# Optimization experiments

Measured on AMD Instinct MI355X. Metric: run time of the kernel, lower is better.

Reference implementation:

```python
import jax, jax.numpy as jnp
import numpy as np
from jax import lax

E = 10        # embed_dim
SEQ = 4000    # input_frame (sample_length=40)
G = 800       # group
F = 5         # frames_in_group
B = 16
VOCAB = 8192


def _conv2d(x, w, b):
    # x: [B, C, H, W], w: [O, I, 3, 3], padding=1 -> SAME
    y = lax.conv_general_dilated(x, w, (1, 1), 'SAME',
                                 dimension_numbers=('NCHW', 'OIHW', 'NCHW'))
    return y + b[None, :, None, None]


def _conv1d_k1(x, w, b):
    # Conv1d(seq, seq, kernel=1): x [B, S, L], w [S_out, S_in]
    return jnp.einsum('oi,bil->bol', w, x) + b[None, :, None]


def _linear(x, w, b):
    # torch Linear: w [out, in]
    return x @ w.T + b


def setup_inputs() -> dict:
    key = jax.random.key(0)
    ks = jax.random.split(key, 24)
    s = 0.02
    inp = {
        'X': jax.random.randint(ks[0], (B, SEQ, 15), 0, VOCAB),
        'emb_table': jax.random.normal(ks[1], (VOCAB, E), jnp.float32),
        'w_dwc_lsp': jax.random.normal(ks[2], (G, G, 3, 3), jnp.float32) * s,
        'b_dwc_lsp': jnp.zeros((G,), jnp.float32),
        'w_dwc_other': jax.random.normal(ks[3], (G, G, 3, 3), jnp.float32) * s,
        'b_dwc_other': jnp.zeros((G,), jnp.float32),
        'w_local': jax.random.normal(ks[4], (SEQ, SEQ), jnp.float32) * s,
        'b_local': jnp.zeros((SEQ,), jnp.float32),
        'w_global': jax.random.normal(ks[5], (SEQ, SEQ), jnp.float32) * s,
        'b_global': jnp.zeros((SEQ,), jnp.float32),
        'w_gq': jax.random.normal(ks[6], (4 * E, 4 * E), jnp.float32) * s,
        'b_gq': jnp.zeros((4 * E,), jnp.float32),
        'w_cq': jax.random.normal(ks[7], (4 * E, 4 * E), jnp.float32) * s,
        'b_cq': jnp.zeros((4 * E,), jnp.float32),
        'w_pq': jax.random.normal(ks[8], (4 * E, 3 * E), jnp.float32) * s,
        'b_pq': jnp.zeros((4 * E,), jnp.float32),
        'w_lk': jax.random.normal(ks[9], (4 * E, 4 * E), jnp.float32) * s,
        'b_lk': jnp.zeros((4 * E,), jnp.float32),
        'w_lv': jax.random.normal(ks[10], (4 * E, 4 * E), jnp.float32) * s,
        'b_lv': jnp.zeros((4 * E,), jnp.float32),
        'w_cls': jax.random.normal(ks[11], (1, SEQ * 4 * E * 3), jnp.float32) * 0.001,
        'b_cls': jnp.zeros((1,), jnp.float32),
        'bn_w': jnp.ones((1,), jnp.float32),
        'bn_b': jnp.zeros((1,), jnp.float32),
    }
    return inp


def reference(X, emb_table, w_dwc_lsp, b_dwc_lsp, w_dwc_other, b_dwc_other,
              w_local, b_local, w_global, b_global,
              w_gq, b_gq, w_cq, b_cq, w_pq, b_pq,
              w_lk, b_lk, w_lv, b_lv, w_cls, b_cls, bn_w, bn_b):
    batch, seq, cw = X.shape
    gamma = jnp.float32(0.8)
    pk = jnp.array([0, 0, 0, 0, 1, 3, 1, 2, 3, 2, 3, 1, 2, 3, 3], jnp.float32)
    D = jnp.repeat(gamma ** pk, E)  # [150]

    Xe = emb_table[X].reshape(batch, seq, cw * E) * D  # [B, S, 150]
    ch = Xe.reshape(batch, seq, cw, E)                  # 15 chunks of E

    lsp = ch[:, :, jnp.array([0, 1, 2, 3])].reshape(batch, seq, 4 * E)
    pitch = ch[:, :, jnp.array([4, 5, 10])].reshape(batch, seq, 3 * E)
    code = ch[:, :, jnp.array([6, 7, 11, 12])].reshape(batch, seq, 4 * E)
    gain = ch[:, :, jnp.array([8, 13, 9, 14])].reshape(batch, seq, 4 * E)

    conv_lsp = _conv2d(lsp.reshape(batch, G, F, 4 * E), w_dwc_lsp, b_dwc_lsp).reshape(batch, seq, 4 * E)
    conv_pitch = _conv2d(pitch.reshape(batch, G, F, 3 * E), w_dwc_other, b_dwc_other).reshape(batch, seq, 3 * E)
    conv_code = _conv2d(code.reshape(batch, G, F, 4 * E), w_dwc_other, b_dwc_other).reshape(batch, seq, 4 * E)
    conv_gain = _conv2d(gain.reshape(batch, G, F, 4 * E), w_dwc_other, b_dwc_other).reshape(batch, seq, 4 * E)

    conv_lsp = _conv1d_k1(conv_lsp, w_local, b_local)
    conv_pitch = _conv1d_k1(conv_pitch, w_local, b_local)
    conv_code = _conv1d_k1(conv_code, w_local, b_local)
    conv_gain = _conv1d_k1(conv_gain, w_local, b_local)

    gain_q = _linear(conv_gain, w_gq, b_gq)    # [B, S, 40]
    pitch_q = _linear(conv_pitch, w_pq, b_pq)  # [B, S, 40]
    code_q = _linear(conv_code, w_cq, b_cq)    # [B, S, 40]
    lsp_k = _linear(conv_lsp, w_lk, b_lk)
    lsp_v = _linear(conv_lsp, w_lv, b_lv)

    # Q @ K^T @ V with no softmax: associate as Q @ (K^T V), O(S*d^2)
    kv = jnp.einsum('bsd,bse->bde', lsp_k, lsp_v)  # [B, 40, 40]
    out_gain = jnp.einsum('bsd,bde->bse', gain_q, kv) + lsp
    out_pitch = jnp.einsum('bsd,bde->bse', pitch_q, kv) + lsp
    out_code = jnp.einsum('bsd,bde->bse', code_q, kv) + lsp

    atten_out = jnp.concatenate([out_gain, out_pitch, out_code], -1)  # [B, S, 120]
    gf = _conv1d_k1(atten_out, w_global, b_global).reshape(batch, -1)  # [B, 480000]

    y = gf @ w_cls.T + b_cls  # [B, 1]
    # BatchNorm1d(1) in eval mode: running_mean=0, running_var=1
    eps = jnp.float32(1e-5)
    y = y * (bn_w / jnp.sqrt(1.0 + eps)) + bn_b
    return jax.nn.sigmoid(y)
```

## Files before the change

kernel.cpp:

```cpp
#include <hip/hip_runtime.h>
#include <hip/hip_bf16.h>

typedef _Float16 f16;
typedef __attribute__((ext_vector_type(8))) _Float16 half8;
typedef __attribute__((ext_vector_type(4))) _Float16 half4;
typedef __attribute__((ext_vector_type(4))) float f32x4;

static const int BN = 16, SEQN = 4000;

__device__ __forceinline__ void gload_lds(f16* lds, const f16* g) {
  __builtin_amdgcn_global_load_lds((const __attribute__((address_space(1))) unsigned int*)g,
                                   (__attribute__((address_space(3))) unsigned int*)lds, 16, 0, 0);
}

__device__ __forceinline__ int xcd_swz(int orig, int nwg) {
  int q = nwg >> 3, r = nwg & 7, x = orig & 7, o = orig >> 3;
  return (x < r ? x * (q + 1) : r * (q + 1) + (x - r) * q) + o;
}

__global__ __launch_bounds__(256) void k_prepA(
    const float* __restrict__ w_dwc_l, f16* __restrict__ wp_lsp,
    const float* __restrict__ w_local, f16* __restrict__ wlp,
    const float* __restrict__ w_cls, f16* __restrict__ wcT) {
  __shared__ float sh[7200];
  int bid = blockIdx.x, t = threadIdx.x;
  if (bid < 800) {
    int o = bid;
    for (int p = t; p < 7200; p += 256) sh[p] = w_dwc_l[(long)o * 7200 + p];
    __syncthreads();
    for (int p = t; p < 7296; p += 256) {
      int seg = p / 2432, r = p - seg * 2432;
      f16 v = (f16)0.f;
      if (r < 2400) { int de = r / 800, gi = r % 800; v = (f16)sh[gi * 9 + seg * 3 + de]; }
      wp_lsp[(long)o * 7296 + p] = v;
    }
  } else if (bid < 4800) {
    int s = bid - 800;
    for (int p = t; p < 4000; p += 256) sh[p] = w_local[(long)s * 4000 + p];
    __syncthreads();
    for (int p = t; p < 4096; p += 256) {
      f16 v = (f16)0.f;
      if (p < 4000) { int f = p / 800, g = p % 800; v = (f16)sh[g * 5 + f]; }
      wlp[(long)s * 4096 + p] = v;
    }
  } else {
    int id = bid - 4800;
    int c0 = (id % 4) * 32, r0 = (id / 4) * 32;
    int tx = t & 31, ty = t >> 5;
    float (*tile)[33] = (float(*)[33])sh;
    for (int i = ty; i < 32; i += 8) {
      int r = r0 + i, c = c0 + tx;
      tile[i][tx] = (r < 4000 && c < 120) ? w_cls[(long)r * 120 + c] : 0.f;
    }
    __syncthreads();
    for (int i = ty; i < 32; i += 8) {
      int c = c0 + i, r = r0 + tx;
      if (c < 128 && r < 4000) wcT[(long)c * 4000 + r] = (f16)(tile[tx][i] * 1024.f);
    }
  }
}

__global__ __launch_bounds__(256) void k_pack_woT(const float* __restrict__ in,
                                                  f16* __restrict__ out) {
  __shared__ float sh[32][289];
  int bg = blockIdx.x % 25, bgi = blockIdx.x / 25;
  int g0 = bg * 32, gi0 = bgi * 32;
  int t = threadIdx.x;
  for (int p = t; p < 32 * 288; p += 256) {
    int gl = p / 288, q = p % 288;
    sh[gl][q] = in[(long)(g0 + gl) * 7200 + gi0 * 9 + q];
  }
  __syncthreads();
  for (int p = t; p < 9 * 32 * 32; p += 256) {
    int gl = p & 31, q = p >> 5;
    int gil = q & 31, z = q >> 5;
    out[(long)z * 640000 + (gi0 + gil) * 800 + g0 + gl] = (f16)sh[gl][gil * 9 + z];
  }
}

__global__ __launch_bounds__(256) void k_gather(
    const int* __restrict__ X, const float* __restrict__ emb,
    f16* __restrict__ P_lsp, f16* __restrict__ P_pit,
    f16* __restrict__ P_cod, f16* __restrict__ P_gai,
    float* __restrict__ lsp32) {
  __shared__ int sx_[2400];
  __shared__ float slsp[6400];
  const float scale[15] = {1.f,1.f,1.f,1.f,0.8f,0.512f,0.8f,0.64f,0.512f,0.64f,0.512f,0.8f,0.64f,0.512f,0.512f};
  const int br[15] = {0,0,0,0,1,1,2,2,3,3,1,2,2,3,3};
  const int po[15] = {0,1,2,3,0,1,0,1,0,2,2,2,3,1,3};
  int bid = blockIdx.x, t = threadIdx.x;
  int b = bid / 25, gc = bid % 25;
  int g0 = gc * 32, s0 = g0 * 5;
  const int* xbase = X + ((long)b * SEQN + s0) * 15;
  for (int p = t; p < 2400; p += 256) sx_[p] = xbase[p];
  __syncthreads();
  for (int it = t; it < 2400; it += 256) {
    int gl = it & 31, q = it >> 5, f = q % 5, c = q / 5;
    int idx = sx_[(gl * 5 + f) * 15 + c];
    const float* er = emb + (long)idx * 10;
    int ty = br[c], p = po[c];
    f16* P = (ty == 0) ? P_lsp : (ty == 1) ? P_pit : (ty == 2) ? P_cod : P_gai;
    int Wp = (ty == 1) ? 32 : 42;
    f16* base = P + ((long)((f + 1) * 16 + b) * Wp + (1 + p * 10)) * 800 + g0 + gl;
    float sc = scale[c];
#pragma unroll
    for (int j = 0; j < 10; j++) {
      float v = er[j] * sc;
      base[(long)j * 800] = (f16)v;
      if (ty == 0) slsp[(gl * 5 + f) * 40 + p * 10 + j] = v;
    }
  }
  __syncthreads();
  float* ldst = lsp32 + ((long)b * SEQN + s0) * 40;
  for (int p = t; p < 6400; p += 256) ldst[p] = slsp[p];
}

__global__ __launch_bounds__(256) void k_c1(const float* __restrict__ wcls,
                                            const float* __restrict__ bg, float* __restrict__ c1p) {
  __shared__ float red[256];
  int t = threadIdx.x;
  float s = 0.f;
  for (long i = (long)blockIdx.x * 256 + t; i < 480000; i += (long)120 * 256)
    s += wcls[i] * bg[i / 120];
  red[t] = s; __syncthreads();
  for (int o = 128; o > 0; o >>= 1) { if (t < o) red[t] += red[t + o]; __syncthreads(); }
  if (t == 0) c1p[blockIdx.x] = red[0];
}

__global__ __launch_bounds__(256) void k_gemm_conv(
    const f16* __restrict__ P, const f16* __restrict__ wp, float* __restrict__ Cp) {
  __shared__ __align__(16) f16 As[2][4096];
  __shared__ __align__(16) f16 Bs[2][4096];
  int lin = xcd_swz(blockIdx.x, 175);
  int nx = lin % 7, my = lin / 7;
  int m0 = my * 128, n0 = nx * 128;
  int z = blockIdx.y;
  int df = z >> 1, hf = z & 1;
  Cp += (long)z * 3200 * 800;
  int t = threadIdx.x;
  int gslot = (t & 3) ^ ((t >> 3) & 3);
  const f16 *ap[2], *bp[2];
#pragma unroll
  for (int q = 0; q < 2; q++) {
    int row = q * 64 + (t >> 2);
    int m = m0 + row;
    int f = m / 640, rem = m % 640, b = rem / 40, e = rem % 40;
    ap[q] = P + ((long)((f + df) * 16 + b) * 42 + e) * 800 + hf * 1216 + gslot * 8;
    bp[q] = wp + (long)(n0 + row) * 7296 + df * 2432 + hf * 1216 + gslot * 8;
  }
  int lane = t & 63, wv = t >> 6, l15 = lane & 15, kg = lane >> 4;
  int wm = (wv >> 1) * 64, wn = (wv & 1) * 64;
  int so = (kg ^ ((l15 >> 1) & 3)) << 3;
  f32x4 acc[4][4] = {};
  gload_lds(&As[0][t * 8], ap[0]); gload_lds(&As[0][2048 + t * 8], ap[1]);
  gload_lds(&Bs[0][t * 8], bp[0]); gload_lds(&Bs[0][2048 + t * 8], bp[1]);
  __syncthreads();
  int cur = 0;
  for (int kt = 0; kt < 38; kt++) {
    if (kt + 1 < 38) {
      int o = (kt + 1) * 32, nb = cur ^ 1;
      gload_lds(&As[nb][t * 8], ap[0] + o); gload_lds(&As[nb][2048 + t * 8], ap[1] + o);
      gload_lds(&Bs[nb][t * 8], bp[0] + o); gload_lds(&Bs[nb][2048 + t * 8], bp[1] + o);
    }
    half8 av[4], bv[4];
#pragma unroll
    for (int i = 0; i < 4; i++) av[i] = *(const half8*)&As[cur][(wm + i * 16 + l15) * 32 + so];
#pragma unroll
    for (int j = 0; j < 4; j++) bv[j] = *(const half8*)&Bs[cur][(wn + j * 16 + l15) * 32 + so];
#pragma unroll
    for (int i = 0; i < 4; i++)
#pragma unroll
      for (int j = 0; j < 4; j++)
        acc[i][j] = __builtin_amdgcn_mfma_f32_16x16x32_f16(av[i], bv[j], acc[i][j], 0, 0, 0);
    __syncthreads();
    cur ^= 1;
  }
#pragma unroll
  for (int i = 0; i < 4; i++) {
    int mb = m0 + wm + i * 16 + kg * 4;
#pragma unroll
    for (int j = 0; j < 4; j++) {
      int n = n0 + wn + j * 16 + l15;
      if (n >= 800) continue;
      f32x4 d = acc[i][j];
#pragma unroll
      for (int r = 0; r < 4; r++)
        Cp[(long)(mb + r) * 800 + n] = d[r];
    }
  }
}

__global__ void k_co_reduce(const float* __restrict__ Cp, const float* __restrict__ bias,
                            f16* __restrict__ co) {
  int id = blockIdx.x * blockDim.x + threadIdx.x;
  if (id >= 640000) return;
  int m = id / 200, n4 = (id % 200) * 4;
  long o = (long)m * 800 + n4;
  f32x4 s = *(const f32x4*)&bias[n4];
#pragma unroll
  for (int z = 0; z < 6; z++) s += *(const f32x4*)&Cp[(long)z * 2560000 + o];
  int f = m / 640, r2 = m % 640;
  half4 h = {(f16)s[0], (f16)s[1], (f16)s[2], (f16)s[3]};
  *(half4*)&co[(long)r2 * 4000 + f * 800 + n4] = h;
}

__global__ __launch_bounds__(256) void k_gemm128(
    const f16* __restrict__ A, int lda, const f16* __restrict__ Bm, int ldb,
    float* __restrict__ C, int ldc,
    int gx, int nwg, int nkt, int KTtot, long cslice, long az, long bz, long cz,
    int Mreal, int Nreal, int Aclamp) {
  __shared__ __align__(16) f16 As[2][4096];
  __shared__ __align__(16) f16 Bs[2][4096];
  A += (long)blockIdx.z * az;
  Bm += (long)blockIdx.z * bz;
  C += (long)blockIdx.z * cz + (long)blockIdx.y * cslice;
  int lin = xcd_swz(blockIdx.x, nwg);
  int nx = lin % gx, my = lin / gx;
  int m0 = my * 128, n0 = nx * 128;
  int kt0 = blockIdx.y * nkt;
  int ktn = nkt; if (kt0 + ktn > KTtot) ktn = KTtot - kt0;
  int t = threadIdx.x;
  int gslot = (t & 3) ^ ((t >> 3) & 3);
  const f16 *ap[2], *bp[2];
#pragma unroll
  for (int q = 0; q < 2; q++) {
    int row = q * 64 + (t >> 2);
    int ra = m0 + row; if (ra >= Aclamp) ra = Aclamp - 1;
    ap[q] = A + (long)ra * lda + (long)kt0 * 32 + gslot * 8;
    bp[q] = Bm + (long)(n0 + row) * ldb + (long)kt0 * 32 + gslot * 8;
  }
  int lane = t & 63, wv = t >> 6, l15 = lane & 15, kg = lane >> 4;
  int wm = (wv >> 1) * 64, wn = (wv & 1) * 64;
  int so = (kg ^ ((l15 >> 1) & 3)) << 3;
  f32x4 acc[4][4] = {};
  gload_lds(&As[0][t * 8], ap[0]); gload_lds(&As[0][2048 + t * 8], ap[1]);
  gload_lds(&Bs[0][t * 8], bp[0]); gload_lds(&Bs[0][2048 + t * 8], bp[1]);
  __syncthreads();
  int cur = 0;
  for (int kt = 0; kt < ktn; kt++) {
    if (kt + 1 < ktn) {
      int o = (kt + 1) * 32, nb = cur ^ 1;
      gload_lds(&As[nb][t * 8], ap[0] + o); gload_lds(&As[nb][2048 + t * 8], ap[1] + o);
      gload_lds(&Bs[nb][t * 8], bp[0] + o); gload_lds(&Bs[nb][2048 + t * 8], bp[1] + o);
    }
    half8 av[4], bv[4];
#pragma unroll
    for (int i = 0; i < 4; i++) av[i] = *(const half8*)&As[cur][(wm + i * 16 + l15) * 32 + so];
#pragma unroll
    for (int j = 0; j < 4; j++) bv[j] = *(const half8*)&Bs[cur][(wn + j * 16 + l15) * 32 + so];
#pragma unroll
    for (int i = 0; i < 4; i++)
#pragma unroll
      for (int j = 0; j < 4; j++)
        acc[i][j] = __builtin_amdgcn_mfma_f32_16x16x32_f16(av[i], bv[j], acc[i][j], 0, 0, 0);
    __syncthreads();
    cur ^= 1;
  }
#pragma unroll
  for (int i = 0; i < 4; i++) {
    int mb = m0 + wm + i * 16 + kg * 4;
#pragma unroll
    for (int j = 0; j < 4; j++) {
      int n = n0 + wn + j * 16 + l15;
      if (n >= Nreal) continue;
      f32x4 d = acc[i][j];
#pragma unroll
      for (int r = 0; r < 4; r++) {
        int m = mb + r;
        if (m >= Mreal) continue;
        C[(long)m * ldc + n] = d[r];
      }
    }
  }
}

__global__ __launch_bounds__(256) void k_gemm_tn(
    const f16* __restrict__ A, int lda, const float* __restrict__ B, int ldb,
    float* __restrict__ C, int ldc, int nkt, int KTtot, long cslice,
    int Mreal, int Nreal) {
  __shared__ __align__(16) f16 As[4096];
  __shared__ __align__(16) f16 Bs[128 * 36];
  int n0 = blockIdx.x * 128;
  int kt0 = blockIdx.y * nkt;
  int ktn = nkt; if (kt0 + ktn > KTtot) ktn = KTtot - kt0;
  C += (long)blockIdx.y * cslice;
  int t = threadIdx.x;
  int gslot = (t & 3) ^ ((t >> 3) & 3);
  const f16 *ap0, *ap1;
  {
    int r0 = t >> 2, r1 = 64 + (t >> 2);
    if (r0 >= Mreal) r0 = Mreal - 1;
    if (r1 >= Mreal) r1 = Mreal - 1;
    ap0 = A + (long)r0 * lda + (long)kt0 * 32 + gslot * 8;
    ap1 = A + (long)r1 * lda + (long)kt0 * 32 + gslot * 8;
  }
  int lane = t & 63, wv = t >> 6;
  int wm = (wv >> 1) * 64, wn = (wv & 1) * 64;
  int l15 = lane & 15, kg = lane >> 4;
  int so = (kg ^ ((l15 >> 1) & 3)) << 3;
  f32x4 acc[4][4] = {};
  for (int kt = 0; kt < ktn; kt++) {
    float rb[4][4];
    int nli[4], kqi[4];
#pragma unroll
    for (int i = 0; i < 4; i++) {
      int id = i * 256 + t;
      nli[i] = id & 127; kqi[i] = id >> 7;
      int gn = n0 + nli[i]; if (gn >= Nreal) gn = Nreal - 1;
      long kb = ((long)(kt0 + kt) * 32 + kqi[i] * 4);
#pragma unroll
      for (int j = 0; j < 4; j++) rb[i][j] = B[(kb + j) * ldb + gn];
    }
    __syncthreads();
    gload_lds(&As[t * 8], ap0 + kt * 32);
    gload_lds(&As[2048 + t * 8], ap1 + kt * 32);
#pragma unroll
    for (int i = 0; i < 4; i++) {
      half4 h = {(f16)rb[i][0], (f16)rb[i][1], (f16)rb[i][2], (f16)rb[i][3]};
      *(half4*)&Bs[nli[i] * 36 + kqi[i] * 4] = h;
    }
    __syncthreads();
    half8 av[4], bv[4];
#pragma unroll
    for (int i = 0; i < 4; i++) {
      av[i] = *(const half8*)(&As[(wm + i * 16 + l15) * 32 + so]);
      bv[i] = *(const half8*)(&Bs[(wn + i * 16 + l15) * 36 + kg * 8]);
    }
#pragma unroll
    for (int i = 0; i < 4; i++)
#pragma unroll
      for (int j = 0; j < 4; j++)
        acc[i][j] = __builtin_amdgcn_mfma_f32_16x16x32_f16(av[i], bv[j], acc[i][j], 0, 0, 0);
  }
#pragma unroll
  for (int i = 0; i < 4; i++) {
    int mb = wm + i * 16 + kg * 4;
#pragma unroll
    for (int j = 0; j < 4; j++) {
      int n = n0 + wn + j * 16 + l15;
      if (n >= Nreal) continue;
      f32x4 d = acc[i][j];
#pragma unroll
      for (int r = 0; r < 4; r++) {
        int m = mb + r;
        if (m >= Mreal) continue;
        C[(long)m * ldc + n] = d[r];
      }
    }
  }
}

template <int MODE>
__global__ __launch_bounds__(128) void k_vredT2(const float* __restrict__ vp,
                                                float* __restrict__ vout,
                                                f16* __restrict__ tout) {
  int s = blockIdx.x * 128 + threadIdx.x;
  int ec = blockIdx.y;
  if (s >= 4000) return;
  int g = s / 5, f = s % 5;
  float sums[40];
#pragma unroll
  for (int eo = 0; eo < 40; eo++) {
    int e = ec * 40 + eo;
    float sum = 0.f;
#pragma unroll
    for (int z = 0; z < 10; z++) sum += vp[(long)z * 480000 + (long)e * 4000 + s];
    sums[eo] = sum;
    if (MODE == 0) tout[(long)e * 4000 + s] = (f16)sum;
    else tout[(long)(f * 120 + e) * 832 + g] = (f16)sum;
  }
#pragma unroll
  for (int q = 0; q < 10; q++)
    *(f32x4*)&vout[(long)s * 120 + ec * 40 + q * 4] = *(f32x4*)&sums[q * 4];
}

__global__ void k_cl_reduce(const float* __restrict__ Clp, const float* __restrict__ bl,
                            float* __restrict__ cl) {
  int id = blockIdx.x * blockDim.x + threadIdx.x;
  if (id >= 640000) return;
  int m = id / 160, n4 = (id % 160) * 4;
  long o = (long)m * 640 + n4;
  f32x4 s = {0.f, 0.f, 0.f, 0.f};
#pragma unroll
  for (int z = 0; z < 6; z++) s += *(const f32x4*)&Clp[(long)z * 2560000 + o];
  float b = bl[m];
  s += (f32x4){b, b, b, b};
  *(f32x4*)&cl[o] = s;
}

__global__ void k_fold_bp(const float* __restrict__ A9, f16* __restrict__ Bp) {
  int id = blockIdx.x * blockDim.x + threadIdx.x;
  if (id >= 7 * 120 * 2496) return;
  int fp = id / 299520;
  int r = id % 299520;
  int eg = r / 2496, k2 = r % 2496;
  int zk = k2 / 832, kk = k2 % 832;
  if (kk >= 800) { Bp[id] = (f16)0.f; return; }
  float s = 0.f;
#pragma unroll
  for (int dh = 0; dh < 3; dh++) {
    int f = fp - dh;
    if (f >= 0 && f < 5)
      s += A9[((long)(dh * 3 + zk) * 640 + f * 120 + eg) * 800 + kk];
  }
  Bp[id] = (f16)s;
}

__global__ __launch_bounds__(256) void k_gemm_u(
    const f16* __restrict__ Pg, const f16* __restrict__ Pp, const f16* __restrict__ Pc,
    const f16* __restrict__ Bp, float* __restrict__ Upart) {
  __shared__ __align__(16) f16 As[2][4096];
  __shared__ __align__(16) f16 Bs[2][4096];
  int m0 = blockIdx.x * 64;
  int y = blockIdx.y, fp = y / 3, zk = y % 3;
  const f16* P; int seg0, jw, Wp, e0;
  if (m0 < 640)       { seg0 = 0;    jw = 40; Wp = 42; e0 = 0;  P = Pg; }
  else if (m0 < 1152) { seg0 = 640;  jw = 30; Wp = 32; e0 = 40; P = Pp; }
  else                { seg0 = 1152; jw = 40; Wp = 42; e0 = 80; P = Pc; }
  P += (long)fp * 16 * Wp * 800;
  int t = threadIdx.x;
  int gslot = (t & 7) ^ ((t >> 3) & 7);
  const f16 *ap[2], *bp[2];
#pragma unroll
  for (int q = 0; q < 2; q++) {
    int row = q * 32 + (t >> 3);
    int l = m0 + row - seg0; if (l >= 16 * jw) l = 0;
    ap[q] = P + ((long)(l / jw) * Wp + (l % jw)) * 800 + (long)zk * 800 + gslot * 8;
    int brow = row; if (e0 + brow > 119) brow = 119 - e0;
    bp[q] = Bp + ((long)fp * 120 + e0 + brow) * 2496 + zk * 832 + gslot * 8;
  }
  int lane = t & 63, wv = t >> 6, l15 = lane & 15, kg = lane >> 4;
  int sx = l15 & 7;
  f32x4 acc[3] = {};
  gload_lds(&As[0][t * 8], ap[0]); gload_lds(&As[0][2048 + t * 8], ap[1]);
  gload_lds(&Bs[0][t * 8], bp[0]); gload_lds(&Bs[0][2048 + t * 8], bp[1]);
  __syncthreads();
  int cur = 0;
  for (int kt = 0; kt < 13; kt++) {
    if (kt + 1 < 13) {
      int o = (kt + 1) * 64, nb = cur ^ 1;
      gload_lds(&As[nb][t * 8], ap[0] + o); gload_lds(&As[nb][2048 + t * 8], ap[1] + o);
      gload_lds(&Bs[nb][t * 8], bp[0] + o); gload_lds(&Bs[nb][2048 + t * 8], bp[1] + o);
    }
#pragma unroll
    for (int ks = 0; ks < 2; ks++) {
      int so = ((ks * 4 + kg) ^ sx) << 3;
      half8 av = *(const half8*)&As[cur][(wv * 16 + l15) * 64 + so];
#pragma unroll
      for (int j = 0; j < 3; j++) {
        half8 bv = *(const half8*)&Bs[cur][(j * 16 + l15) * 64 + so];
        acc[j] = __builtin_amdgcn_mfma_f32_16x16x32_f16(av, bv, acc[j], 0, 0, 0);
      }
    }
    __syncthreads();
    cur ^= 1;
  }
#pragma unroll
  for (int j = 0; j < 3; j++) {
    int n = j * 16 + l15;
    if (n >= 40) continue;
    f32x4 d = acc[j];
#pragma unroll
    for (int r = 0; r < 4; r++) {
      int m = m0 + wv * 16 + kg * 4 + r;
      if (m - seg0 >= 16 * jw) continue;
      Upart[((long)y * 1792 + m) * 40 + n] = d[r];
    }
  }
}

__global__ void k_ured(const float* __restrict__ Upart, const float* __restrict__ cbblv,
                       float* __restrict__ Ufin) {
  int id = blockIdx.x * blockDim.x + threadIdx.x;
  if (id >= 1792 * 40) return;
  int m = id / 40, e = id % 40;
  int e0 = m < 640 ? 0 : (m < 1152 ? 40 : 80);
  float s = cbblv[e0 + e];
  for (int y = 0; y < 21; y++) s += Upart[(long)y * 71680 + id];
  Ufin[id] = s;
}

__global__ __launch_bounds__(256) void k_consts(
    const float* __restrict__ Vt, const float* __restrict__ vmat,
    const float* __restrict__ bconv, const float* __restrict__ blocal,
    float* __restrict__ cbblv, float* __restrict__ svv) {
  __shared__ float r1[256], r2[256];
  int e = blockIdx.x, t = threadIdx.x;
  float a = 0.f, b = 0.f;
  for (int s = t; s < 4000; s += 256) {
    a += bconv[s / 5] * Vt[(long)s * 120 + e] + blocal[s] * vmat[(long)s * 120 + e];
    b += vmat[(long)s * 120 + e];
  }
  r1[t] = a; r2[t] = b; __syncthreads();
  for (int o = 128; o > 0; o >>= 1) {
    if (t < o) { r1[t] += r1[t + o]; r2[t] += r2[t + o]; }
    __syncthreads();
  }
  if (t == 0) { cbblv[e] = r1[0]; svv[e] = r2[0]; }
}

__global__ __launch_bounds__(256) void k_kv_partial(
    const float* __restrict__ cl, const float* __restrict__ wlk, const float* __restrict__ blk,
    const float* __restrict__ wlv, const float* __restrict__ blv, float* __restrict__ kvp) {
  __shared__ float s_wk[1600], s_wv[1600];
  __shared__ float s_cl[8][40], s_k[8][40], s_v[8][40];
  int t = threadIdx.x, chunk = blockIdx.x, b = blockIdx.y;
  for (int p = t; p < 1600; p += 256) { s_wk[p] = wlk[p]; s_wv[p] = wlv[p]; }
  float acc[7] = {0.f, 0.f, 0.f, 0.f, 0.f, 0.f, 0.f};
  for (int c8 = 0; c8 < 20; c8++) {
    int sb = chunk * 160 + c8 * 8;
    __syncthreads();
    for (int p = t; p < 320; p += 256) {
      int sl = p / 40, e = p % 40;
      s_cl[sl][e] = cl[(long)(sb + sl) * 640 + b * 40 + e];
    }
    __syncthreads();
    for (int p = t; p < 640; p += 256) {
      int half = p / 320, q = p % 320, sl = q / 40, d = q % 40;
      const float* w = half ? s_wv : s_wk;
      float r = half ? blv[d] : blk[d];
      for (int e = 0; e < 40; e++) r += w[d * 40 + e] * s_cl[sl][e];
      if (half) s_v[sl][d] = r; else s_k[sl][d] = r;
    }
    __syncthreads();
    int ai = 0;
    for (int p = t; p < 1600; p += 256, ai++) {
      int d = p / 40, e = p % 40;
      float a = acc[ai];
      for (int sl = 0; sl < 8; sl++) a += s_k[sl][d] * s_v[sl][e];
      acc[ai] = a;
    }
  }
  int ai = 0;
  for (int p = t; p < 1600; p += 256, ai++)
    kvp[((long)(b * 25 + chunk)) * 1600 + p] = acc[ai];
}

__global__ void k_kv_reduce(const float* __restrict__ kvp, float* __restrict__ kv) {
  int i = blockIdx.x * blockDim.x + threadIdx.x;
  if (i >= 16 * 1600) return;
  int b = i / 1600, p = i % 1600;
  float s = 0.f;
  for (int c = 0; c < 25; c++) s += kvp[((long)(b * 25 + c)) * 1600 + p];
  kv[i] = s;
}

__global__ __launch_bounds__(256) void k_resid(
    const float* __restrict__ lsp32, const float* __restrict__ vmat,
    float* __restrict__ rpart) {
  __shared__ float red[256];
  int chunk = blockIdx.x, b = blockIdx.y, t = threadIdx.x;
  int s0 = chunk * 160;
  float y = 0.f;
  for (int idx = t; idx < 1600; idx += 256) {
    int sr = idx / 10, d4 = idx % 10;
    const float* lp = lsp32 + ((long)b * SEQN + s0 + sr) * 40 + d4 * 4;
    const float* vp = vmat + (long)(s0 + sr) * 120 + d4 * 4;
    f32x4 l = *(const f32x4*)lp;
    f32x4 vs = *(const f32x4*)vp + *(const f32x4*)(vp + 40) + *(const f32x4*)(vp + 80);
    y += l[0] * vs[0] + l[1] * vs[1] + l[2] * vs[2] + l[3] * vs[3];
  }
  red[t] = y; __syncthreads();
  for (int o = 128; o > 0; o >>= 1) { if (t < o) red[t] += red[t + o]; __syncthreads(); }
  if (t == 0) rpart[b * 25 + chunk] = red[0];
}

__global__ __launch_bounds__(256) void k_final(
    const float* __restrict__ Ufin, const float* __restrict__ kvb,
    const float* __restrict__ rpart,
    const float* __restrict__ wgq, const float* __restrict__ wpq, const float* __restrict__ wcq,
    const float* __restrict__ bgq, const float* __restrict__ bpq, const float* __restrict__ bcq,
    const float* __restrict__ svv, const float* __restrict__ c1p,
    const float* __restrict__ bcls, const float* __restrict__ bnw,
    const float* __restrict__ bnb, float* __restrict__ out) {
  __shared__ float s_kv[1600], s_U[4800], s_w[4400], s_bq[120], s_sv[120], s_red[256];
  int b = blockIdx.x, t = threadIdx.x;
  for (int p = t; p < 1600; p += 256) {
    s_kv[p] = kvb[b * 1600 + p];
    s_w[p] = wgq[p];
    s_w[2800 + p] = wcq[p];
  }
  for (int p = t; p < 1200; p += 256) s_w[1600 + p] = wpq[p];
  for (int p = t; p < 4800; p += 256) {
    int tt = p / 1600, r = p % 1600, j = r / 40, e = r % 40;
    float uv = 0.f;
    if (tt == 0) uv = Ufin[(b * 40 + j) * 40 + e];
    else if (tt == 1) { if (j < 30) uv = Ufin[(640 + b * 30 + j) * 40 + e]; }
    else uv = Ufin[(1152 + b * 40 + j) * 40 + e];
    s_U[p] = uv;
  }
  if (t < 40) { s_bq[t] = bgq[t]; s_bq[40 + t] = bpq[t]; s_bq[80 + t] = bcq[t]; }
  for (int p = t; p < 120; p += 256) s_sv[p] = svv[p];
  __syncthreads();
  float y = 0.f;
  for (int p = t; p < 4800; p += 256) {
    int tt = p / 1600, q = p % 1600, d = q / 40, e = q % 40;
    float T = 0.f;
    if (tt == 0) {
      for (int j = 0; j < 40; j++) T += s_w[d * 40 + j] * s_U[j * 40 + e];
    } else if (tt == 1) {
      for (int j = 0; j < 30; j++) T += s_w[1600 + d * 30 + j] * s_U[1600 + j * 40 + e];
    } else {
      for (int j = 0; j < 40; j++) T += s_w[2800 + d * 40 + j] * s_U[3200 + j * 40 + e];
    }
    y += s_kv[d * 40 + e] * (T + s_bq[tt * 40 + d] * s_sv[tt * 40 + e]);
  }
  for (int p = t; p < 25; p += 256) y += rpart[b * 25 + p];
  s_red[t] = y; __syncthreads();
  for (int o = 128; o > 0; o >>= 1) { if (t < o) s_red[t] += s_red[t + o]; __syncthreads(); }
  if (t == 0) {
    float c1 = bcls[0];
    for (int i = 0; i < 120; i++) c1 += c1p[i];
    float yy = s_red[0] * (1.f / 1024.f) + c1;
    yy = yy * (bnw[0] * rsqrtf(1.f + 1e-5f)) + bnb[0];
    out[b] = 1.f / (1.f + expf(-yy));
  }
}

extern "C" void kernel_launch(void* const* d_in, const int* in_sizes, int n_in,
                              void* d_out, int out_size, void* d_ws, size_t ws_size,
                              hipStream_t stream) {
  const int*   X        = (const int*)d_in[0];
  const float* emb      = (const float*)d_in[1];
  const float* w_dwc_l  = (const float*)d_in[2];
  const float* b_dwc_l  = (const float*)d_in[3];
  const float* w_dwc_o  = (const float*)d_in[4];
  const float* b_dwc_o  = (const float*)d_in[5];
  const float* w_local  = (const float*)d_in[6];
  const float* b_local  = (const float*)d_in[7];
  const float* w_global = (const float*)d_in[8];
  const float* b_global = (const float*)d_in[9];
  const float* w_gq = (const float*)d_in[10];
  const float* b_gq = (const float*)d_in[11];
  const float* w_cq = (const float*)d_in[12];
  const float* b_cq = (const float*)d_in[13];
  const float* w_pq = (const float*)d_in[14];
  const float* b_pq = (const float*)d_in[15];
  const float* w_lk = (const float*)d_in[16];
  const float* b_lk = (const float*)d_in[17];
  const float* w_lv = (const float*)d_in[18];
  const float* b_lv = (const float*)d_in[19];
  const float* w_cls = (const float*)d_in[20];
  const float* b_cls = (const float*)d_in[21];
  const float* bn_w = (const float*)d_in[22];
  const float* bn_b = (const float*)d_in[23];
  float* out = (float*)d_out;

  char* ws = (char*)d_ws;
  size_t off = 0;
  auto alloc = [&](size_t bytes) -> void* {
    off = (off + 255) & ~(size_t)255;
    void* p = ws + off; off += bytes; return p;
  };

  const size_t sz_p40 = (size_t)7 * 16 * 42 * 800 * 2;
  const size_t sz_p30 = (size_t)7 * 16 * 32 * 800 * 2;
  f16* P_lsp = (f16*)alloc(sz_p40 + 256);
  f16* P_pit = (f16*)alloc(sz_p30 + 256);
  f16* P_cod = (f16*)alloc(sz_p40 + 256);
  f16* P_gai = (f16*)alloc(sz_p40 + 256);
  float* lsp32 = (float*)alloc((size_t)16 * 4000 * 40 * 4);
  f16* wp_lsp = (f16*)alloc((size_t)896 * 7296 * 2);
  f16* wlp    = (f16*)alloc((size_t)4000 * 4096 * 2 + 256);
  f16* wcT    = (f16*)alloc((size_t)128 * 4000 * 2);
  f16* vT     = (f16*)alloc((size_t)128 * 4000 * 2);
  f16* co     = (f16*)alloc((size_t)640 * 4000 * 2 + 256);
  float* cl   = (float*)alloc((size_t)4000 * 640 * 4);
  float* vmat  = (float*)alloc((size_t)480000 * 4);
  float* Vt    = (float*)alloc((size_t)480000 * 4);
  f16* vtT   = (f16*)alloc((size_t)640 * 832 * 2 + 256);
  f16* Bp    = (f16*)alloc((size_t)7 * 120 * 2496 * 2);
  float* Upart = (float*)alloc((size_t)21 * 1792 * 40 * 4);
  float* Ufin  = (float*)alloc((size_t)1792 * 40 * 4);
  float* cbblv = (float*)alloc(120 * 4);
  float* svv   = (float*)alloc(120 * 4);
  float* kvp  = (float*)alloc((size_t)400 * 1600 * 4);
  float* kvb  = (float*)alloc((size_t)16 * 1600 * 4);
  float* c1p  = (float*)alloc(120 * 4);
  float* rpart = (float*)alloc(400 * 4);
  char* arena = (char*)alloc((size_t)64 * 1024 * 1024);
  float* A9   = (float*)arena;
  f16*   woT  = (f16*)(arena + 18500000);
  float* vpart = (float*)(arena + 30200000);
  float* Cp   = (float*)arena;
  float* Clp  = (float*)arena;
  (void)ws_size; (void)in_sizes; (void)n_in; (void)out_size;

  hipMemsetAsync(P_lsp, 0, sz_p40, stream);
  hipMemsetAsync(P_pit, 0, sz_p30, stream);
  hipMemsetAsync(P_cod, 0, sz_p40, stream);
  hipMemsetAsync(P_gai, 0, sz_p40, stream);
  hipMemsetAsync(vtT, 0, (size_t)640 * 832 * 2, stream);

  k_prepA<<<5300, 256, 0, stream>>>(w_dwc_l, wp_lsp, w_local, wlp, w_cls, wcT);
  k_pack_woT<<<625, 256, 0, stream>>>(w_dwc_o, woT);
  k_gather<<<400, 256, 0, stream>>>(X, emb, P_lsp, P_pit, P_cod, P_gai, lsp32);
  k_c1<<<120, 256, 0, stream>>>(w_cls, b_global, c1p);

  {
    dim3 g(32, 10);
    k_gemm_tn<<<g, 256, 0, stream>>>(wcT, 4000, w_global, 4000, vpart, 4000,
                                     13, 125, 480000, 120, 4000);
  }
  {
    dim3 g(32, 3);
    k_vredT2<0><<<g, 128, 0, stream>>>(vpart, vmat, vT);
  }

  {
    dim3 g(32, 10);
    k_gemm_tn<<<g, 256, 0, stream>>>(vT, 4000, w_local, 4000, vpart, 4000,
                                     13, 125, 480000, 120, 4000);
  }
  {
    dim3 g(32, 3);
    k_vredT2<1><<<g, 128, 0, stream>>>(vpart, Vt, vtT);
  }

  k_consts<<<120, 256, 0, stream>>>(Vt, vmat, b_dwc_o, b_local, cbblv, svv);

  {
    dim3 g(25, 16);
    k_resid<<<g, 256, 0, stream>>>(lsp32, vmat, rpart);
  }

  {
    dim3 g(35, 1, 9);
    k_gemm128<<<g, 256, 0, stream>>>(vtT, 832, woT, 800, A9, 800,
                                     7, 35, 26, 26, 0, 0, 640000, 512000, 600, 800, 600);
  }
  k_fold_bp<<<8190, 256, 0, stream>>>(A9, Bp);

  {
    dim3 g(175, 6);
    k_gemm_conv<<<g, 256, 0, stream>>>(P_lsp, wp_lsp, Cp);
  }
  k_co_reduce<<<2500, 256, 0, stream>>>(Cp, b_dwc_l, co);

  {
    dim3 g(160, 6);
    k_gemm128<<<g, 256, 0, stream>>>(wlp, 4096, co, 4000, Clp, 640,
                                     5, 160, 22, 128, 2560000L, 0, 0, 0, 4000, 640, 4000);
  }
  k_cl_reduce<<<2500, 256, 0, stream>>>(Clp, b_local, cl);

  {
    dim3 g(25, 16);
    k_kv_partial<<<g, 256, 0, stream>>>(cl, w_lk, b_lk, w_lv, b_lv, kvp);
  }
  k_kv_reduce<<<100, 256, 0, stream>>>(kvp, kvb);

  {
    dim3 g(28, 21);
    k_gemm_u<<<g, 256, 0, stream>>>(P_gai, P_pit, P_cod, Bp, Upart);
  }
  k_ured<<<280, 256, 0, stream>>>(Upart, cbblv, Ufin);

  k_final<<<16, 256, 0, stream>>>(Ufin, kvb, rpart,
                                  w_gq, w_pq, w_cq, b_gq, b_pq, b_cq,
                                  svv, c1p, b_cls, bn_w, bn_b, out);
}
```

Measured before the change: 501.4 us.

## Merge independent kernels into phase kernels and rebalance split-K partitions

Independent stages are packed into nine phase kernels, each dispatching on block index to a different device-side body. This cuts the launch count and lets unrelated work (conv GEMM with the global TN GEMM, the reductions, the kv and A9 work) run concurrently on the GPU. The conv GEMM split drops from 6 to 3 slices with twice the K loop, and the local GEMM drops from 6 to 4 split-K slices, so the reduction kernels read fewer partials. Buffers that used to alias in one arena now get their own allocations, so phases that run together do not overwrite each other. The cost is fewer blocks per GEMM and shared-memory sizing set by the largest body in each phase.

Result: faster. 468.5 us (-6.6%).

```diff
diff --git a/kernel.cpp b/kernel.cpp
--- a/kernel.cpp
+++ b/kernel.cpp
@@ -18,12 +18,12 @@
   return (x < r ? x * (q + 1) : r * (q + 1) + (x - r) * q) + o;
 }
 
-__global__ __launch_bounds__(256) void k_prepA(
+__device__ __forceinline__ void body_prepA(char* SM, int bid,
     const float* __restrict__ w_dwc_l, f16* __restrict__ wp_lsp,
     const float* __restrict__ w_local, f16* __restrict__ wlp,
     const float* __restrict__ w_cls, f16* __restrict__ wcT) {
-  __shared__ float sh[7200];
-  int bid = blockIdx.x, t = threadIdx.x;
+  float* sh = (float*)SM;
+  int t = threadIdx.x;
   if (bid < 800) {
     int o = bid;
     for (int p = t; p < 7200; p += 256) sh[p] = w_dwc_l[(long)o * 7200 + p];
@@ -47,7 +47,7 @@
     int id = bid - 4800;
     int c0 = (id % 4) * 32, r0 = (id / 4) * 32;
     int tx = t & 31, ty = t >> 5;
-    float (*tile)[33] = (float(*)[33])sh;
+    float (*tile)[33] = (float(*)[33])SM;
     for (int i = ty; i < 32; i += 8) {
       int r = r0 + i, c = c0 + tx;
       tile[i][tx] = (r < 4000 && c < 120) ? w_cls[(long)r * 120 + c] : 0.f;
@@ -60,10 +60,10 @@
   }
 }
 
-__global__ __launch_bounds__(256) void k_pack_woT(const float* __restrict__ in,
-                                                  f16* __restrict__ out) {
-  __shared__ float sh[32][289];
-  int bg = blockIdx.x % 25, bgi = blockIdx.x / 25;
+__device__ __forceinline__ void body_woT(char* SM, int id,
+    const float* __restrict__ in, f16* __restrict__ out) {
+  float (*sh)[289] = (float(*)[289])SM;
+  int bg = id % 25, bgi = id / 25;
   int g0 = bg * 32, gi0 = bgi * 32;
   int t = threadIdx.x;
   for (int p = t; p < 32 * 288; p += 256) {
@@ -78,17 +78,17 @@
   }
 }
 
-__global__ __launch_bounds__(256) void k_gather(
+__device__ __forceinline__ void body_gather(char* SM, int bid,
     const int* __restrict__ X, const float* __restrict__ emb,
     f16* __restrict__ P_lsp, f16* __restrict__ P_pit,
     f16* __restrict__ P_cod, f16* __restrict__ P_gai,
     float* __restrict__ lsp32) {
-  __shared__ int sx_[2400];
-  __shared__ float slsp[6400];
+  int* sx_ = (int*)SM;
+  float* slsp = (float*)(SM + 9600);
   const float scale[15] = {1.f,1.f,1.f,1.f,0.8f,0.512f,0.8f,0.64f,0.512f,0.64f,0.512f,0.8f,0.64f,0.512f,0.512f};
   const int br[15] = {0,0,0,0,1,1,2,2,3,3,1,2,2,3,3};
   const int po[15] = {0,1,2,3,0,1,0,1,0,2,2,2,3,1,3};
-  int bid = blockIdx.x, t = threadIdx.x;
+  int t = threadIdx.x;
   int b = bid / 25, gc = bid % 25;
   int g0 = gc * 32, s0 = g0 * 5;
   const int* xbase = X + ((long)b * SEQN + s0) * 15;
@@ -115,27 +115,27 @@
   for (int p = t; p < 6400; p += 256) ldst[p] = slsp[p];
 }
 
-__global__ __launch_bounds__(256) void k_c1(const float* __restrict__ wcls,
-                                            const float* __restrict__ bg, float* __restrict__ c1p) {
-  __shared__ float red[256];
+__device__ __forceinline__ void body_c1(char* SM, int blk,
+    const float* __restrict__ wcls, const float* __restrict__ bg,
+    float* __restrict__ c1p) {
+  float* red = (float*)SM;
   int t = threadIdx.x;
   float s = 0.f;
-  for (long i = (long)blockIdx.x * 256 + t; i < 480000; i += (long)120 * 256)
+  for (long i = (long)blk * 256 + t; i < 480000; i += (long)120 * 256)
     s += wcls[i] * bg[i / 120];
   red[t] = s; __syncthreads();
   for (int o = 128; o > 0; o >>= 1) { if (t < o) red[t] += red[t + o]; __syncthreads(); }
-  if (t == 0) c1p[blockIdx.x] = red[0];
-}
-
-__global__ __launch_bounds__(256) void k_gemm_conv(
+  if (t == 0) c1p[blk] = red[0];
+}
+
+__device__ __forceinline__ void body_conv(char* SM, int id,
     const f16* __restrict__ P, const f16* __restrict__ wp, float* __restrict__ Cp) {
-  __shared__ __align__(16) f16 As[2][4096];
-  __shared__ __align__(16) f16 Bs[2][4096];
-  int lin = xcd_swz(blockIdx.x, 175);
+  f16* Asb = (f16*)SM;
+  f16* Bsb = Asb + 8192;
+  int lin = xcd_swz(id % 175, 175);
+  int z = id / 175;
   int nx = lin % 7, my = lin / 7;
   int m0 = my * 128, n0 = nx * 128;
-  int z = blockIdx.y;
-  int df = z >> 1, hf = z & 1;
   Cp += (long)z * 3200 * 800;
   int t = threadIdx.x;
   int gslot = (t & 3) ^ ((t >> 3) & 3);
@@ -145,28 +145,28 @@
     int row = q * 64 + (t >> 2);
     int m = m0 + row;
     int f = m / 640, rem = m % 640, b = rem / 40, e = rem % 40;
-    ap[q] = P + ((long)((f + df) * 16 + b) * 42 + e) * 800 + hf * 1216 + gslot * 8;
-    bp[q] = wp + (long)(n0 + row) * 7296 + df * 2432 + hf * 1216 + gslot * 8;
+    ap[q] = P + ((long)((f + z) * 16 + b) * 42 + e) * 800 + gslot * 8;
+    bp[q] = wp + (long)(n0 + row) * 7296 + z * 2432 + gslot * 8;
   }
   int lane = t & 63, wv = t >> 6, l15 = lane & 15, kg = lane >> 4;
   int wm = (wv >> 1) * 64, wn = (wv & 1) * 64;
   int so = (kg ^ ((l15 >> 1) & 3)) << 3;
   f32x4 acc[4][4] = {};
-  gload_lds(&As[0][t * 8], ap[0]); gload_lds(&As[0][2048 + t * 8], ap[1]);
-  gload_lds(&Bs[0][t * 8], bp[0]); gload_lds(&Bs[0][2048 + t * 8], bp[1]);
+  gload_lds(&Asb[t * 8], ap[0]); gload_lds(&Asb[2048 + t * 8], ap[1]);
+  gload_lds(&Bsb[t * 8], bp[0]); gload_lds(&Bsb[2048 + t * 8], bp[1]);
   __syncthreads();
   int cur = 0;
-  for (int kt = 0; kt < 38; kt++) {
-    if (kt + 1 < 38) {
+  for (int kt = 0; kt < 76; kt++) {
+    if (kt + 1 < 76) {
       int o = (kt + 1) * 32, nb = cur ^ 1;
-      gload_lds(&As[nb][t * 8], ap[0] + o); gload_lds(&As[nb][2048 + t * 8], ap[1] + o);
-      gload_lds(&Bs[nb][t * 8], bp[0] + o); gload_lds(&Bs[nb][2048 + t * 8], bp[1] + o);
+      gload_lds(&Asb[nb * 4096 + t * 8], ap[0] + o); gload_lds(&Asb[nb * 4096 + 2048 + t * 8], ap[1] + o);
+      gload_lds(&Bsb[nb * 4096 + t * 8], bp[0] + o); gload_lds(&Bsb[nb * 4096 + 2048 + t * 8], bp[1] + o);
     }
     half8 av[4], bv[4];
 #pragma unroll
-    for (int i = 0; i < 4; i++) av[i] = *(const half8*)&As[cur][(wm + i * 16 + l15) * 32 + so];
-#pragma unroll
-    for (int j = 0; j < 4; j++) bv[j] = *(const half8*)&Bs[cur][(wn + j * 16 + l15) * 32 + so];
+    for (int i = 0; i < 4; i++) av[i] = *(const half8*)&Asb[cur * 4096 + (wm + i * 16 + l15) * 32 + so];
+#pragma unroll
+    for (int j = 0; j < 4; j++) bv[j] = *(const half8*)&Bsb[cur * 4096 + (wn + j * 16 + l15) * 32 + so];
 #pragma unroll
     for (int i = 0; i < 4; i++)
 #pragma unroll
@@ -190,34 +190,20 @@
   }
 }
 
-__global__ void k_co_reduce(const float* __restrict__ Cp, const float* __restrict__ bias,
-                            f16* __restrict__ co) {
-  int id = blockIdx.x * blockDim.x + threadIdx.x;
-  if (id >= 640000) return;
-  int m = id / 200, n4 = (id % 200) * 4;
-  long o = (long)m * 800 + n4;
-  f32x4 s = *(const f32x4*)&bias[n4];
-#pragma unroll
-  for (int z = 0; z < 6; z++) s += *(const f32x4*)&Cp[(long)z * 2560000 + o];
-  int f = m / 640, r2 = m % 640;
-  half4 h = {(f16)s[0], (f16)s[1], (f16)s[2], (f16)s[3]};
-  *(half4*)&co[(long)r2 * 4000 + f * 800 + n4] = h;
-}
-
-__global__ __launch_bounds__(256) void k_gemm128(
+__device__ __forceinline__ void body_gemm128(char* SM, int x, int ky, int z,
     const f16* __restrict__ A, int lda, const f16* __restrict__ Bm, int ldb,
     float* __restrict__ C, int ldc,
     int gx, int nwg, int nkt, int KTtot, long cslice, long az, long bz, long cz,
     int Mreal, int Nreal, int Aclamp) {
-  __shared__ __align__(16) f16 As[2][4096];
-  __shared__ __align__(16) f16 Bs[2][4096];
-  A += (long)blockIdx.z * az;
-  Bm += (long)blockIdx.z * bz;
-  C += (long)blockIdx.z * cz + (long)blockIdx.y * cslice;
-  int lin = xcd_swz(blockIdx.x, nwg);
+  f16* Asb = (f16*)SM;
+  f16* Bsb = Asb + 8192;
+  A += (long)z * az;
+  Bm += (long)z * bz;
+  C += (long)z * cz + (long)ky * cslice;
+  int lin = xcd_swz(x, nwg);
   int nx = lin % gx, my = lin / gx;
   int m0 = my * 128, n0 = nx * 128;
-  int kt0 = blockIdx.y * nkt;
+  int kt0 = ky * nkt;
   int ktn = nkt; if (kt0 + ktn > KTtot) ktn = KTtot - kt0;
   int t = threadIdx.x;
   int gslot = (t & 3) ^ ((t >> 3) & 3);
@@ -233,21 +219,21 @@
   int wm = (wv >> 1) * 64, wn = (wv & 1) * 64;
   int so = (kg ^ ((l15 >> 1) & 3)) << 3;
   f32x4 acc[4][4] = {};
-  gload_lds(&As[0][t * 8], ap[0]); gload_lds(&As[0][2048 + t * 8], ap[1]);
-  gload_lds(&Bs[0][t * 8], bp[0]); gload_lds(&Bs[0][2048 + t * 8], bp[1]);
+  gload_lds(&Asb[t * 8], ap[0]); gload_lds(&Asb[2048 + t * 8], ap[1]);
+  gload_lds(&Bsb[t * 8], bp[0]); gload_lds(&Bsb[2048 + t * 8], bp[1]);
   __syncthreads();
   int cur = 0;
   for (int kt = 0; kt < ktn; kt++) {
     if (kt + 1 < ktn) {
       int o = (kt + 1) * 32, nb = cur ^ 1;
-      gload_lds(&As[nb][t * 8], ap[0] + o); gload_lds(&As[nb][2048 + t * 8], ap[1] + o);
-      gload_lds(&Bs[nb][t * 8], bp[0] + o); gload_lds(&Bs[nb][2048 + t * 8], bp[1] + o);
+      gload_lds(&Asb[nb * 4096 + t * 8], ap[0] + o); gload_lds(&Asb[nb * 4096 + 2048 + t * 8], ap[1] + o);
+      gload_lds(&Bsb[nb * 4096 + t * 8], bp[0] + o); gload_lds(&Bsb[nb * 4096 + 2048 + t * 8], bp[1] + o);
     }
     half8 av[4], bv[4];
 #pragma unroll
-    for (int i = 0; i < 4; i++) av[i] = *(const half8*)&As[cur][(wm + i * 16 + l15) * 32 + so];
-#pragma unroll
-    for (int j = 0; j < 4; j++) bv[j] = *(const half8*)&Bs[cur][(wn + j * 16 + l15) * 32 + so];
+    for (int i = 0; i < 4; i++) av[i] = *(const half8*)&Asb[cur * 4096 + (wm + i * 16 + l15) * 32 + so];
+#pragma unroll
+    for (int j = 0; j < 4; j++) bv[j] = *(const half8*)&Bsb[cur * 4096 + (wn + j * 16 + l15) * 32 + so];
 #pragma unroll
     for (int i = 0; i < 4; i++)
 #pragma unroll
@@ -274,16 +260,17 @@
   }
 }
 
-__global__ __launch_bounds__(256) void k_gemm_tn(
+__device__ __forceinline__ void body_tn(char* SM, int id,
     const f16* __restrict__ A, int lda, const float* __restrict__ B, int ldb,
     float* __restrict__ C, int ldc, int nkt, int KTtot, long cslice,
     int Mreal, int Nreal) {
-  __shared__ __align__(16) f16 As[4096];
-  __shared__ __align__(16) f16 Bs[128 * 36];
-  int n0 = blockIdx.x * 128;
-  int kt0 = blockIdx.y * nkt;
+  f16* As = (f16*)SM;
+  f16* Bs = As + 4096;
+  int n0 = (id & 31) * 128;
+  int ky = id >> 5;
+  int kt0 = ky * nkt;
   int ktn = nkt; if (kt0 + ktn > KTtot) ktn = KTtot - kt0;
-  C += (long)blockIdx.y * cslice;
+  C += (long)ky * cslice;
   int t = threadIdx.x;
   int gslot = (t & 3) ^ ((t >> 3) & 3);
   const f16 *ap0, *ap1;
@@ -304,8 +291,8 @@
     int nli[4], kqi[4];
 #pragma unroll
     for (int i = 0; i < 4; i++) {
-      int id = i * 256 + t;
-      nli[i] = id & 127; kqi[i] = id >> 7;
+      int idd = i * 256 + t;
+      nli[i] = idd & 127; kqi[i] = idd >> 7;
       int gn = n0 + nli[i]; if (gn >= Nreal) gn = Nreal - 1;
       long kb = ((long)(kt0 + kt) * 32 + kqi[i] * 4);
 #pragma unroll
@@ -350,12 +337,23 @@
   }
 }
 
-template <int MODE>
-__global__ __launch_bounds__(128) void k_vredT2(const float* __restrict__ vp,
-                                                float* __restrict__ vout,
-                                                f16* __restrict__ tout) {
-  int s = blockIdx.x * 128 + threadIdx.x;
-  int ec = blockIdx.y;
+__device__ __forceinline__ void body_co_red(long gid,
+    const float* __restrict__ Cp, const float* __restrict__ bias, f16* __restrict__ co) {
+  if (gid >= 640000) return;
+  int m = gid / 200, n4 = (gid % 200) * 4;
+  long o = (long)m * 800 + n4;
+  f32x4 s = *(const f32x4*)&bias[n4];
+#pragma unroll
+  for (int z = 0; z < 3; z++) s += *(const f32x4*)&Cp[(long)z * 2560000 + o];
+  int f = m / 640, r2 = m % 640;
+  half4 h = {(f16)s[0], (f16)s[1], (f16)s[2], (f16)s[3]};
+  *(half4*)&co[(long)r2 * 4000 + f * 800 + n4] = h;
+}
+
+__device__ __forceinline__ void body_vred(int idb, int MODE,
+    const float* __restrict__ vp, float* __restrict__ vout, f16* __restrict__ tout) {
+  int x = idb & 15, ec = idb >> 4;
+  int s = x * 256 + threadIdx.x;
   if (s >= 4000) return;
   int g = s / 5, f = s % 5;
   float sums[40];
@@ -374,182 +372,24 @@
     *(f32x4*)&vout[(long)s * 120 + ec * 40 + q * 4] = *(f32x4*)&sums[q * 4];
 }
 
-__global__ void k_cl_reduce(const float* __restrict__ Clp, const float* __restrict__ bl,
-                            float* __restrict__ cl) {
-  int id = blockIdx.x * blockDim.x + threadIdx.x;
-  if (id >= 640000) return;
-  int m = id / 160, n4 = (id % 160) * 4;
+__device__ __forceinline__ void body_cl_red(long gid,
+    const float* __restrict__ Clp, const float* __restrict__ bl, float* __restrict__ cl) {
+  if (gid >= 640000) return;
+  int m = gid / 160, n4 = (gid % 160) * 4;
   long o = (long)m * 640 + n4;
   f32x4 s = {0.f, 0.f, 0.f, 0.f};
 #pragma unroll
-  for (int z = 0; z < 6; z++) s += *(const f32x4*)&Clp[(long)z * 2560000 + o];
+  for (int z = 0; z < 4; z++) s += *(const f32x4*)&Clp[(long)z * 2560000 + o];
   float b = bl[m];
   s += (f32x4){b, b, b, b};
   *(f32x4*)&cl[o] = s;
 }
 
-__global__ void k_fold_bp(const float* __restrict__ A9, f16* __restrict__ Bp) {
-  int id = blockIdx.x * blockDim.x + threadIdx.x;
-  if (id >= 7 * 120 * 2496) return;
-  int fp = id / 299520;
-  int r = id % 299520;
-  int eg = r / 2496, k2 = r % 2496;
-  int zk = k2 / 832, kk = k2 % 832;
-  if (kk >= 800) { Bp[id] = (f16)0.f; return; }
-  float s = 0.f;
-#pragma unroll
-  for (int dh = 0; dh < 3; dh++) {
-    int f = fp - dh;
-    if (f >= 0 && f < 5)
-      s += A9[((long)(dh * 3 + zk) * 640 + f * 120 + eg) * 800 + kk];
-  }
-  Bp[id] = (f16)s;
-}
-
-__global__ __launch_bounds__(256) void k_gemm_u(
-    const f16* __restrict__ Pg, const f16* __restrict__ Pp, const f16* __restrict__ Pc,
-    const f16* __restrict__ Bp, float* __restrict__ Upart) {
-  __shared__ __align__(16) f16 As[2][4096];
-  __shared__ __align__(16) f16 Bs[2][4096];
-  int m0 = blockIdx.x * 64;
-  int y = blockIdx.y, fp = y / 3, zk = y % 3;
-  const f16* P; int seg0, jw, Wp, e0;
-  if (m0 < 640)       { seg0 = 0;    jw = 40; Wp = 42; e0 = 0;  P = Pg; }
-  else if (m0 < 1152) { seg0 = 640;  jw = 30; Wp = 32; e0 = 40; P = Pp; }
-  else                { seg0 = 1152; jw = 40; Wp = 42; e0 = 80; P = Pc; }
-  P += (long)fp * 16 * Wp * 800;
-  int t = threadIdx.x;
-  int gslot = (t & 7) ^ ((t >> 3) & 7);
-  const f16 *ap[2], *bp[2];
-#pragma unroll
-  for (int q = 0; q < 2; q++) {
-    int row = q * 32 + (t >> 3);
-    int l = m0 + row - seg0; if (l >= 16 * jw) l = 0;
-    ap[q] = P + ((long)(l / jw) * Wp + (l % jw)) * 800 + (long)zk * 800 + gslot * 8;
-    int brow = row; if (e0 + brow > 119) brow = 119 - e0;
-    bp[q] = Bp + ((long)fp * 120 + e0 + brow) * 2496 + zk * 832 + gslot * 8;
-  }
-  int lane = t & 63, wv = t >> 6, l15 = lane & 15, kg = lane >> 4;
-  int sx = l15 & 7;
-  f32x4 acc[3] = {};
-  gload_lds(&As[0][t * 8], ap[0]); gload_lds(&As[0][2048 + t * 8], ap[1]);
-  gload_lds(&Bs[0][t * 8], bp[0]); gload_lds(&Bs[0][2048 + t * 8], bp[1]);
-  __syncthreads();
-  int cur = 0;
-  for (int kt = 0; kt < 13; kt++) {
-    if (kt + 1 < 13) {
-      int o = (kt + 1) * 64, nb = cur ^ 1;
-      gload_lds(&As[nb][t * 8], ap[0] + o); gload_lds(&As[nb][2048 + t * 8], ap[1] + o);
-      gload_lds(&Bs[nb][t * 8], bp[0] + o); gload_lds(&Bs[nb][2048 + t * 8], bp[1] + o);
-    }
-#pragma unroll
-    for (int ks = 0; ks < 2; ks++) {
-      int so = ((ks * 4 + kg) ^ sx) << 3;
-      half8 av = *(const half8*)&As[cur][(wv * 16 + l15) * 64 + so];
-#pragma unroll
-      for (int j = 0; j < 3; j++) {
-        half8 bv = *(const half8*)&Bs[cur][(j * 16 + l15) * 64 + so];
-        acc[j] = __builtin_amdgcn_mfma_f32_16x16x32_f16(av, bv, acc[j], 0, 0, 0);
-      }
-    }
-    __syncthreads();
-    cur ^= 1;
-  }
-#pragma unroll
-  for (int j = 0; j < 3; j++) {
-    int n = j * 16 + l15;
-    if (n >= 40) continue;
-    f32x4 d = acc[j];
-#pragma unroll
-    for (int r = 0; r < 4; r++) {
-      int m = m0 + wv * 16 + kg * 4 + r;
-      if (m - seg0 >= 16 * jw) continue;
-      Upart[((long)y * 1792 + m) * 40 + n] = d[r];
-    }
-  }
-}
-
-__global__ void k_ured(const float* __restrict__ Upart, const float* __restrict__ cbblv,
-                       float* __restrict__ Ufin) {
-  int id = blockIdx.x * blockDim.x + threadIdx.x;
-  if (id >= 1792 * 40) return;
-  int m = id / 40, e = id % 40;
-  int e0 = m < 640 ? 0 : (m < 1152 ? 40 : 80);
-  float s = cbblv[e0 + e];
-  for (int y = 0; y < 21; y++) s += Upart[(long)y * 71680 + id];
-  Ufin[id] = s;
-}
-
-__global__ __launch_bounds__(256) void k_consts(
-    const float* __restrict__ Vt, const float* __restrict__ vmat,
-    const float* __restrict__ bconv, const float* __restrict__ blocal,
-    float* __restrict__ cbblv, float* __restrict__ svv) {
-  __shared__ float r1[256], r2[256];
-  int e = blockIdx.x, t = threadIdx.x;
-  float a = 0.f, b = 0.f;
-  for (int s = t; s < 4000; s += 256) {
-    a += bconv[s / 5] * Vt[(long)s * 120 + e] + blocal[s] * vmat[(long)s * 120 + e];
-    b += vmat[(long)s * 120 + e];
-  }
-  r1[t] = a; r2[t] = b; __syncthreads();
-  for (int o = 128; o > 0; o >>= 1) {
-    if (t < o) { r1[t] += r1[t + o]; r2[t] += r2[t + o]; }
-    __syncthreads();
-  }
-  if (t == 0) { cbblv[e] = r1[0]; svv[e] = r2[0]; }
-}
-
-__global__ __launch_bounds__(256) void k_kv_partial(
-    const float* __restrict__ cl, const float* __restrict__ wlk, const float* __restrict__ blk,
-    const float* __restrict__ wlv, const float* __restrict__ blv, float* __restrict__ kvp) {
-  __shared__ float s_wk[1600], s_wv[1600];
-  __shared__ float s_cl[8][40], s_k[8][40], s_v[8][40];
-  int t = threadIdx.x, chunk = blockIdx.x, b = blockIdx.y;
-  for (int p = t; p < 1600; p += 256) { s_wk[p] = wlk[p]; s_wv[p] = wlv[p]; }
-  float acc[7] = {0.f, 0.f, 0.f, 0.f, 0.f, 0.f, 0.f};
-  for (int c8 = 0; c8 < 20; c8++) {
-    int sb = chunk * 160 + c8 * 8;
-    __syncthreads();
-    for (int p = t; p < 320; p += 256) {
-      int sl = p / 40, e = p % 40;
-      s_cl[sl][e] = cl[(long)(sb + sl) * 640 + b * 40 + e];
-    }
-    __syncthreads();
-    for (int p = t; p < 640; p += 256) {
-      int half = p / 320, q = p % 320, sl = q / 40, d = q % 40;
-      const float* w = half ? s_wv : s_wk;
-      float r = half ? blv[d] : blk[d];
-      for (int e = 0; e < 40; e++) r += w[d * 40 + e] * s_cl[sl][e];
-      if (half) s_v[sl][d] = r; else s_k[sl][d] = r;
-    }
-    __syncthreads();
-    int ai = 0;
-    for (int p = t; p < 1600; p += 256, ai++) {
-      int d = p / 40, e = p % 40;
-      float a = acc[ai];
-      for (int sl = 0; sl < 8; sl++) a += s_k[sl][d] * s_v[sl][e];
-      acc[ai] = a;
-    }
-  }
-  int ai = 0;
-  for (int p = t; p < 1600; p += 256, ai++)
-    kvp[((long)(b * 25 + chunk)) * 1600 + p] = acc[ai];
-}
-
-__global__ void k_kv_reduce(const float* __restrict__ kvp, float* __restrict__ kv) {
-  int i = blockIdx.x * blockDim.x + threadIdx.x;
-  if (i >= 16 * 1600) return;
-  int b = i / 1600, p = i % 1600;
-  float s = 0.f;
-  for (int c = 0; c < 25; c++) s += kvp[((long)(b * 25 + c)) * 1600 + p];
-  kv[i] = s;
-}
-
-__global__ __launch_bounds__(256) void k_resid(
+__device__ __forceinline__ void body_resid(char* SM, int chunk, int b,
     const float* __restrict__ lsp32, const float* __restrict__ vmat,
     float* __restrict__ rpart) {
-  __shared__ float red[256];
-  int chunk = blockIdx.x, b = blockIdx.y, t = threadIdx.x;
+  float* red = (float*)SM;
+  int t = threadIdx.x;
   int s0 = chunk * 160;
   float y = 0.f;
   for (int idx = t; idx < 1600; idx += 256) {
@@ -563,6 +403,251 @@
   red[t] = y; __syncthreads();
   for (int o = 128; o > 0; o >>= 1) { if (t < o) red[t] += red[t + o]; __syncthreads(); }
   if (t == 0) rpart[b * 25 + chunk] = red[0];
+}
+
+__device__ __forceinline__ void body_kv(char* SM, int chunk, int b,
+    const float* __restrict__ cl, const float* __restrict__ wlk, const float* __restrict__ blk,
+    const float* __restrict__ wlv, const float* __restrict__ blv, float* __restrict__ kvp) {
+  float* s_wk = (float*)SM;
+  float* s_wv = s_wk + 1600;
+  float* s_cl = s_wv + 1600;
+  float* s_k  = s_cl + 320;
+  float* s_v  = s_k + 320;
+  int t = threadIdx.x;
+  for (int p = t; p < 1600; p += 256) { s_wk[p] = wlk[p]; s_wv[p] = wlv[p]; }
+  float acc[7] = {0.f, 0.f, 0.f, 0.f, 0.f, 0.f, 0.f};
+  for (int c8 = 0; c8 < 20; c8++) {
+    int sb = chunk * 160 + c8 * 8;
+    __syncthreads();
+    for (int p = t; p < 320; p += 256) {
+      int sl = p / 40, e = p % 40;
+      s_cl[sl * 40 + e] = cl[(long)(sb + sl) * 640 + b * 40 + e];
+    }
+    __syncthreads();
+    for (int p = t; p < 640; p += 256) {
+      int half = p / 320, q = p % 320, sl = q / 40, d = q % 40;
+      const float* w = half ? s_wv : s_wk;
+      float r = half ? blv[d] : blk[d];
+      for (int e = 0; e < 40; e++) r += w[d * 40 + e] * s_cl[sl * 40 + e];
+      if (half) s_v[sl * 40 + d] = r; else s_k[sl * 40 + d] = r;
+    }
+    __syncthreads();
+    int ai = 0;
+    for (int p = t; p < 1600; p += 256, ai++) {
+      int d = p / 40, e = p % 40;
+      float a = acc[ai];
+      for (int sl = 0; sl < 8; sl++) a += s_k[sl * 40 + d] * s_v[sl * 40 + e];
+      acc[ai] = a;
+    }
+  }
+  int ai = 0;
+  for (int p = t; p < 1600; p += 256, ai++)
+    kvp[((long)(b * 25 + chunk)) * 1600 + p] = acc[ai];
+}
+
+__device__ __forceinline__ void body_consts(char* SM, int e,
+    const float* __restrict__ Vt, const float* __restrict__ vmat,
+    const float* __restrict__ bconv, const float* __restrict__ blocal,
+    float* __restrict__ cbblv, float* __restrict__ svv) {
+  float* r1 = (float*)SM;
+  float* r2 = r1 + 256;
+  int t = threadIdx.x;
+  float a = 0.f, b = 0.f;
+  for (int s = t; s < 4000; s += 256) {
+    a += bconv[s / 5] * Vt[(long)s * 120 + e] + blocal[s] * vmat[(long)s * 120 + e];
+    b += vmat[(long)s * 120 + e];
+  }
+  r1[t] = a; r2[t] = b; __syncthreads();
+  for (int o = 128; o > 0; o >>= 1) {
+    if (t < o) { r1[t] += r1[t + o]; r2[t] += r2[t + o]; }
+    __syncthreads();
+  }
+  if (t == 0) { cbblv[e] = r1[0]; svv[e] = r2[0]; }
+}
+
+__device__ __forceinline__ void body_fold(long gid,
+    const float* __restrict__ A9, f16* __restrict__ Bp) {
+  if (gid >= 7 * 120 * 2496) return;
+  int fp = gid / 299520;
+  int r = gid % 299520;
+  int eg = r / 2496, k2 = r % 2496;
+  int zk = k2 / 832, kk = k2 % 832;
+  if (kk >= 800) { Bp[gid] = (f16)0.f; return; }
+  float s = 0.f;
+#pragma unroll
+  for (int dh = 0; dh < 3; dh++) {
+    int f = fp - dh;
+    if (f >= 0 && f < 5)
+      s += A9[((long)(dh * 3 + zk) * 640 + f * 120 + eg) * 800 + kk];
+  }
+  Bp[gid] = (f16)s;
+}
+
+__device__ __forceinline__ void body_kvred(long gid,
+    const float* __restrict__ kvp, float* __restrict__ kv) {
+  if (gid >= 16 * 1600) return;
+  int b = gid / 1600, p = gid % 1600;
+  float s = 0.f;
+  for (int c = 0; c < 25; c++) s += kvp[((long)(b * 25 + c)) * 1600 + p];
+  kv[gid] = s;
+}
+
+__device__ __forceinline__ void body_U(char* SM, int id,
+    const f16* __restrict__ Pg, const f16* __restrict__ Pp, const f16* __restrict__ Pc,
+    const f16* __restrict__ Bp, float* __restrict__ Upart) {
+  f16* Asb = (f16*)SM;
+  f16* Bsb = Asb + 8192;
+  int m0 = (id % 28) * 64;
+  int y = id / 28, fp = y / 3, zk = y % 3;
+  const f16* P; int seg0, jw, Wp, e0;
+  if (m0 < 640)       { seg0 = 0;    jw = 40; Wp = 42; e0 = 0;  P = Pg; }
+  else if (m0 < 1152) { seg0 = 640;  jw = 30; Wp = 32; e0 = 40; P = Pp; }
+  else                { seg0 = 1152; jw = 40; Wp = 42; e0 = 80; P = Pc; }
+  P += (long)fp * 16 * Wp * 800;
+  int t = threadIdx.x;
+  int gslot = (t & 7) ^ ((t >> 3) & 7);
+  const f16 *ap[2], *bp[2];
+#pragma unroll
+  for (int q = 0; q < 2; q++) {
+    int row = q * 32 + (t >> 3);
+    int l = m0 + row - seg0; if (l >= 16 * jw) l = 0;
+    ap[q] = P + ((long)(l / jw) * Wp + (l % jw)) * 800 + (long)zk * 800 + gslot * 8;
+    int brow = row; if (e0 + brow > 119) brow = 119 - e0;
+    bp[q] = Bp + ((long)fp * 120 + e0 + brow) * 2496 + zk * 832 + gslot * 8;
+  }
+  int lane = t & 63, wv = t >> 6, l15 = lane & 15, kg = lane >> 4;
+  int sx = l15 & 7;
+  f32x4 acc[3] = {};
+  gload_lds(&Asb[t * 8], ap[0]); gload_lds(&Asb[2048 + t * 8], ap[1]);
+  gload_lds(&Bsb[t * 8], bp[0]); gload_lds(&Bsb[2048 + t * 8], bp[1]);
+  __syncthreads();
+  int cur = 0;
+  for (int kt = 0; kt < 13; kt++) {
+    if (kt + 1 < 13) {
+      int o = (kt + 1) * 64, nb = cur ^ 1;
+      gload_lds(&Asb[nb * 4096 + t * 8], ap[0] + o); gload_lds(&Asb[nb * 4096 + 2048 + t * 8], ap[1] + o);
+      gload_lds(&Bsb[nb * 4096 + t * 8], bp[0] + o); gload_lds(&Bsb[nb * 4096 + 2048 + t * 8], bp[1] + o);
+    }
+#pragma unroll
+    for (int ks = 0; ks < 2; ks++) {
+      int so = ((ks * 4 + kg) ^ sx) << 3;
+      half8 av = *(const half8*)&Asb[cur * 4096 + (wv * 16 + l15) * 64 + so];
+#pragma unroll
+      for (int j = 0; j < 3; j++) {
+        half8 bv = *(const half8*)&Bsb[cur * 4096 + (j * 16 + l15) * 64 + so];
+        acc[j] = __builtin_amdgcn_mfma_f32_16x16x32_f16(av, bv, acc[j], 0, 0, 0);
+      }
+    }
+    __syncthreads();
+    cur ^= 1;
+  }
+#pragma unroll
+  for (int j = 0; j < 3; j++) {
+    int n = j * 16 + l15;
+    if (n >= 40) continue;
+    f32x4 d = acc[j];
+#pragma unroll
+    for (int r = 0; r < 4; r++) {
+      int m = m0 + wv * 16 + kg * 4 + r;
+      if (m - seg0 >= 16 * jw) continue;
+      Upart[((long)y * 1792 + m) * 40 + n] = d[r];
+    }
+  }
+}
+
+__device__ __forceinline__ void body_ured(long gid,
+    const float* __restrict__ Upart, const float* __restrict__ cbblv,
+    float* __restrict__ Ufin) {
+  if (gid >= 1792 * 40) return;
+  int m = gid / 40, e = gid % 40;
+  int e0 = m < 640 ? 0 : (m < 1152 ? 40 : 80);
+  float s = cbblv[e0 + e];
+  for (int y = 0; y < 21; y++) s += Upart[(long)y * 71680 + gid];
+  Ufin[gid] = s;
+}
+
+__global__ __launch_bounds__(256) void k_phase0(
+    const float* w_dwc_l, f16* wp_lsp, const float* w_local, f16* wlp,
+    const float* w_cls, f16* wcT, const float* w_dwc_o, f16* woT,
+    const int* X, const float* emb, f16* P_lsp, f16* P_pit, f16* P_cod, f16* P_gai,
+    float* lsp32, const float* b_global, float* c1p) {
+  __shared__ __align__(16) char SM[37120];
+  int bid = blockIdx.x;
+  if (bid < 5300) body_prepA(SM, bid, w_dwc_l, wp_lsp, w_local, wlp, w_cls, wcT);
+  else if (bid < 5925) body_woT(SM, bid - 5300, w_dwc_o, woT);
+  else if (bid < 6325) body_gather(SM, bid - 5925, X, emb, P_lsp, P_pit, P_cod, P_gai, lsp32);
+  else body_c1(SM, bid - 6325, w_cls, b_global, c1p);
+}
+
+__global__ __launch_bounds__(256) void k_phase1(
+    const f16* P_lsp, const f16* wp_lsp, float* Cp,
+    const f16* wcT, const float* w_global, float* vpart) {
+  __shared__ __align__(16) char SM[32768];
+  int bid = blockIdx.x;
+  if (bid < 525) body_conv(SM, bid, P_lsp, wp_lsp, Cp);
+  else body_tn(SM, bid - 525, wcT, 4000, w_global, 4000, vpart, 4000, 13, 125, 480000L, 120, 4000);
+}
+
+__global__ __launch_bounds__(256) void k_phase2(
+    const float* Cp, const float* b_dwc_l, f16* co,
+    const float* vpart, float* vmat, f16* vT) {
+  int bid = blockIdx.x;
+  if (bid < 2500) body_co_red((long)bid * 256 + threadIdx.x, Cp, b_dwc_l, co);
+  else body_vred(bid - 2500, 0, vpart, vmat, vT);
+}
+
+__global__ __launch_bounds__(256) void k_phase3(
+    const f16* wlp, const f16* co, float* Clp,
+    const f16* vT, const float* w_local, float* vpart) {
+  __shared__ __align__(16) char SM[32768];
+  int bid = blockIdx.x;
+  if (bid < 640) body_gemm128(SM, bid % 160, bid / 160, 0, wlp, 4096, co, 4000, Clp, 640,
+                              5, 160, 32, 128, 2560000L, 0, 0, 0, 4000, 640, 4000);
+  else body_tn(SM, bid - 640, vT, 4000, w_local, 4000, vpart, 4000, 13, 125, 480000L, 120, 4000);
+}
+
+__global__ __launch_bounds__(256) void k_phase4(
+    const float* Clp, const float* b_local, float* cl,
+    const float* vpart, float* Vt, f16* vtT,
+    const float* lsp32, const float* vmat, float* rpart) {
+  __shared__ __align__(16) char SM[1024];
+  int bid = blockIdx.x;
+  if (bid < 2500) body_cl_red((long)bid * 256 + threadIdx.x, Clp, b_local, cl);
+  else if (bid < 2548) body_vred(bid - 2500, 1, vpart, Vt, vtT);
+  else { int id = bid - 2548; body_resid(SM, id % 25, id / 25, lsp32, vmat, rpart); }
+}
+
+__global__ __launch_bounds__(256) void k_phase5(
+    const float* cl, const float* w_lk, const float* b_lk,
+    const float* w_lv, const float* b_lv, float* kvp,
+    const f16* vtT, const f16* woT, float* A9,
+    const float* Vt, const float* vmat, const float* b_dwc_o, const float* b_local,
+    float* cbblv, float* svv) {
+  __shared__ __align__(16) char SM[32768];
+  int bid = blockIdx.x;
+  if (bid < 400) body_kv(SM, bid % 25, bid / 25, cl, w_lk, b_lk, w_lv, b_lv, kvp);
+  else if (bid < 715) { int id = bid - 400; body_gemm128(SM, id % 35, 0, id / 35, vtT, 832, woT, 800, A9, 800,
+                                                          7, 35, 26, 26, 0L, 0, 640000, 512000, 600, 800, 600); }
+  else body_consts(SM, bid - 715, Vt, vmat, b_dwc_o, b_local, cbblv, svv);
+}
+
+__global__ __launch_bounds__(256) void k_phase6(
+    const float* A9, f16* Bp, const float* kvp, float* kvb) {
+  int bid = blockIdx.x;
+  if (bid < 8190) body_fold((long)bid * 256 + threadIdx.x, A9, Bp);
+  else body_kvred((long)(bid - 8190) * 256 + threadIdx.x, kvp, kvb);
+}
+
+__global__ __launch_bounds__(256) void k_phase7(
+    const f16* P_gai, const f16* P_pit, const f16* P_cod,
+    const f16* Bp, float* Upart) {
+  __shared__ __align__(16) char SM[32768];
+  body_U(SM, blockIdx.x, P_gai, P_pit, P_cod, Bp, Upart);
+}
+
+__global__ __launch_bounds__(256) void k_phase8(
+    const float* Upart, const float* cbblv, float* Ufin) {
+  body_ured((long)blockIdx.x * 256 + threadIdx.x, Upart, cbblv, Ufin);
 }
 
 __global__ __launch_bounds__(256) void k_final(
@@ -678,12 +763,12 @@
   float* kvb  = (float*)alloc((size_t)16 * 1600 * 4);
   float* c1p  = (float*)alloc(120 * 4);
   float* rpart = (float*)alloc(400 * 4);
-  char* arena = (char*)alloc((size_t)64 * 1024 * 1024);
-  float* A9   = (float*)arena;
-  f16*   woT  = (f16*)(arena + 18500000);
-  float* vpart = (float*)(arena + 30200000);
-  float* Cp   = (float*)arena;
-  float* Clp  = (float*)arena;
+  f16* woT = (f16*)alloc(((size_t)9 * 640000 + 76800) * 2);
+  float* vpart = (float*)alloc((size_t)10 * 480000 * 4);
+  char* arena = (char*)alloc((size_t)41 * 1024 * 1024);
+  float* Cp  = (float*)arena;
+  float* Clp = (float*)arena;
+  float* A9  = (float*)arena;
   (void)ws_size; (void)in_sizes; (void)n_in; (void)out_size;
 
   hipMemsetAsync(P_lsp, 0, sz_p40, stream);
@@ -692,70 +777,18 @@
   hipMemsetAsync(P_gai, 0, sz_p40, stream);
   hipMemsetAsync(vtT, 0, (size_t)640 * 832 * 2, stream);
 
-  k_prepA<<<5300, 256, 0, stream>>>(w_dwc_l, wp_lsp, w_local, wlp, w_cls, wcT);
-  k_pack_woT<<<625, 256, 0, stream>>>(w_dwc_o, woT);
-  k_gather<<<400, 256, 0, stream>>>(X, emb, P_lsp, P_pit, P_cod, P_gai, lsp32);
-  k_c1<<<120, 256, 0, stream>>>(w_cls, b_global, c1p);
-
-  {
-    dim3 g(32, 10);
-    k_gemm_tn<<<g, 256, 0, stream>>>(wcT, 4000, w_global, 4000, vpart, 4000,
-                                     13, 125, 480000, 120, 4000);
-  }
-  {
-    dim3 g(32, 3);
-    k_vredT2<0><<<g, 128, 0, stream>>>(vpart, vmat, vT);
-  }
-
-  {
-    dim3 g(32, 10);
-    k_gemm_tn<<<g, 256, 0, stream>>>(vT, 4000, w_local, 4000, vpart, 4000,
-                                     13, 125, 480000, 120, 4000);
-  }
-  {
-    dim3 g(32, 3);
-    k_vredT2<1><<<g, 128, 0, stream>>>(vpart, Vt, vtT);
-  }
-
-  k_consts<<<120, 256, 0, stream>>>(Vt, vmat, b_dwc_o, b_local, cbblv, svv);
-
-  {
-    dim3 g(25, 16);
-    k_resid<<<g, 256, 0, stream>>>(lsp32, vmat, rpart);
-  }
-
-  {
-    dim3 g(35, 1, 9);
-    k_gemm128<<<g, 256, 0, stream>>>(vtT, 832, woT, 800, A9, 800,
-                                     7, 35, 26, 26, 0, 0, 640000, 512000, 600, 800, 600);
-  }
-  k_fold_bp<<<8190, 256, 0, stream>>>(A9, Bp);
-
-  {
-    dim3 g(175, 6);
-    k_gemm_conv<<<g, 256, 0, stream>>>(P_lsp, wp_lsp, Cp);
-  }
-  k_co_reduce<<<2500, 256, 0, stream>>>(Cp, b_dwc_l, co);
-
-  {
-    dim3 g(160, 6);
-    k_gemm128<<<g, 256, 0, stream>>>(wlp, 4096, co, 4000, Clp, 640,
-                                     5, 160, 22, 128, 2560000L, 0, 0, 0, 4000, 640, 4000);
-  }
-  k_cl_reduce<<<2500, 256, 0, stream>>>(Clp, b_local, cl);
-
-  {
-    dim3 g(25, 16);
-    k_kv_partial<<<g, 256, 0, stream>>>(cl, w_lk, b_lk, w_lv, b_lv, kvp);
-  }
-  k_kv_reduce<<<100, 256, 0, stream>>>(kvp, kvb);
-
-  {
-    dim3 g(28, 21);
-    k_gemm_u<<<g, 256, 0, stream>>>(P_gai, P_pit, P_cod, Bp, Upart);
-  }
-  k_ured<<<280, 256, 0, stream>>>(Upart, cbblv, Ufin);
-
+  k_phase0<<<6445, 256, 0, stream>>>(w_dwc_l, wp_lsp, w_local, wlp, w_cls, wcT,
+                                     w_dwc_o, woT, X, emb, P_lsp, P_pit, P_cod, P_gai,
+                                     lsp32, b_global, c1p);
+  k_phase1<<<845, 256, 0, stream>>>(P_lsp, wp_lsp, Cp, wcT, w_global, vpart);
+  k_phase2<<<2548, 256, 0, stream>>>(Cp, b_dwc_l, co, vpart, vmat, vT);
+  k_phase3<<<960, 256, 0, stream>>>(wlp, co, Clp, vT, w_local, vpart);
+  k_phase4<<<2948, 256, 0, stream>>>(Clp, b_local, cl, vpart, Vt, vtT, lsp32, vmat, rpart);
+  k_phase5<<<835, 256, 0, stream>>>(cl, w_lk, b_lk, w_lv, b_lv, kvp,
+                                    vtT, woT, A9, Vt, vmat, b_dwc_o, b_local, cbblv, svv);
+  k_phase6<<<8290, 256, 0, stream>>>(A9, Bp, kvp, kvb);
+  k_phase7<<<588, 256, 0, stream>>>(P_gai, P_pit, P_cod, Bp, Upart);
+  k_phase8<<<280, 256, 0, stream>>>(Upart, cbblv, Ufin);
   k_final<<<16, 256, 0, stream>>>(Ufin, kvb, rpart,
                                   w_gq, w_pq, w_cq, b_gq, b_pq, b_cq,
                                   svv, c1p, b_cls, bn_w, bn_b, out);
```
